# Performance work log

Hardware: AMD Instinct MI355X
Metric: run time of the kernel (lower is better)

The kernel has to match this reference:

```python
import jax, jax.numpy as jnp
import numpy as np

B, NQ, NK = 4, 2048, 2048
D_MODEL, D_K, D_V, H = 1024, 1024, 1024, 16


def setup_inputs() -> dict:
    key = jax.random.key(0)
    ks = jax.random.split(key, 8)
    return {
        "queries": jax.random.normal(ks[0], (B, NQ, D_MODEL), dtype=jnp.float32),
        "keys": jax.random.normal(ks[1], (B, NK, D_MODEL), dtype=jnp.float32),
        "values": jax.random.normal(ks[2], (B, NK, D_MODEL), dtype=jnp.float32),
        # nn.Linear weights init.normal_(std=0.001); stored here in (in, out) layout
        "Wq": jax.random.normal(ks[3], (D_MODEL, D_K), dtype=jnp.float32) * 0.001,
        "Wk": jax.random.normal(ks[4], (D_MODEL, D_K), dtype=jnp.float32) * 0.001,
        "Wv": jax.random.normal(ks[5], (D_MODEL, D_V), dtype=jnp.float32) * 0.001,
        "Wo": jax.random.normal(ks[6], (D_V, D_MODEL), dtype=jnp.float32) * 0.001,
        "bo": jnp.zeros((D_MODEL,), dtype=jnp.float32),
    }


def reference(queries, keys, values, Wq, Wk, Wv, Wo, bo):
    b_s, nq, _ = queries.shape
    nk = keys.shape[1]
    hd_k = D_K // H  # per-head key dim
    hd_v = D_V // H  # per-head value dim
    # projections -> [b, h, n, hd]
    q = (queries @ Wq).reshape(b_s, nq, H, hd_k).transpose(0, 2, 1, 3)
    k = (keys @ Wk).reshape(b_s, nk, H, hd_k).transpose(0, 2, 1, 3)
    v = (values @ Wv).reshape(b_s, nk, H, hd_v).transpose(0, 2, 1, 3)
    # NOTE: original scales by sqrt(d_k) (full d_k), not per-head dim
    att = jnp.einsum("bhqd,bhkd->bhqk", q, k) / np.float32(np.sqrt(D_K))
    att = jax.nn.softmax(att, axis=-1)
    # dropout = identity (eval mode)
    out = jnp.einsum("bhqk,bhkd->bhqd", att, v)
    out = out.transpose(0, 2, 1, 3).reshape(b_s, nq, D_V)
    return out @ Wo + bo
```

## Files before the change

kernel.cpp:

```cpp
#include <hip/hip_runtime.h>


#define DM    1024
#define NSEQ  2048
#define HEADS 16
#define HD    64

typedef float floatx4 __attribute__((ext_vector_type(4)));
typedef short s16x4   __attribute__((ext_vector_type(4)));
typedef short s16x8   __attribute__((ext_vector_type(8)));
typedef unsigned int u32x4 __attribute__((ext_vector_type(4)));

static __device__ __forceinline__ floatx4 mfma_bf16(s16x8 a, s16x8 b, floatx4 c) {
  return __builtin_amdgcn_mfma_f32_16x16x32_bf16(a, b, c, 0, 0, 0);
}

static __device__ __forceinline__ void gload_lds16(const void* g, void* l) {
  __builtin_amdgcn_global_load_lds(
      (const __attribute__((address_space(1))) unsigned*)g,
      (__attribute__((address_space(3))) unsigned*)l, 16, 0, 0);
}

static __device__ __forceinline__ unsigned lds_addr(const void* p) {
  return (unsigned)(unsigned long long)p;
}

static __device__ __forceinline__ s16x8 ds_read_b128a(unsigned byteaddr) {
  s16x8 r;
  asm volatile("ds_read_b128 %0, %1" : "=v"(r) : "v"(byteaddr));
  return r;
}

#define WAIT_LGKM0() \
  { asm volatile("s_waitcnt lgkmcnt(0)" ::: "memory"); __builtin_amdgcn_sched_barrier(0); }
#define WAIT_VMCNT(N) asm volatile("s_waitcnt vmcnt(" #N ")" ::: "memory")

static __device__ __forceinline__ short f2bf(float f) {
  unsigned u = __builtin_bit_cast(unsigned, f);
  u += 0x7FFFu + ((u >> 16) & 1u);
  return (short)(u >> 16);
}

static __device__ __forceinline__ unsigned cvtpk_bf16(float lo, float hi) {
  unsigned r;
  asm("v_cvt_pk_bf16_f32 %0, %1, %2" : "=v"(r) : "v"(lo), "v"(hi));
  return r;
}

static __device__ __forceinline__ unsigned pack2_bf16(float a, float b) {
  unsigned ua = __builtin_bit_cast(unsigned, a) + 0x8000u;
  unsigned ub = __builtin_bit_cast(unsigned, b) + 0x8000u;
#if __has_builtin(__builtin_amdgcn_perm)
  return __builtin_amdgcn_perm(ub, ua, 0x07060302u);
#else
  return (ub & 0xffff0000u) | (ua >> 16);
#endif
}

__global__ __launch_bounds__(256) void transpose_cast_w(
    const float* __restrict__ W0, const float* __restrict__ W1,
    const float* __restrict__ W2, const float* __restrict__ W3,
    short* __restrict__ T0, short* __restrict__ T1,
    short* __restrict__ T2, short* __restrict__ T3) {
  __shared__ float tile[32][33];
  const float* W = blockIdx.z == 0 ? W0 : blockIdx.z == 1 ? W1 : blockIdx.z == 2 ? W2 : W3;
  short*       T = blockIdx.z == 0 ? T0 : blockIdx.z == 1 ? T1 : blockIdx.z == 2 ? T2 : T3;
  const int bx = blockIdx.x * 32;
  const int by = blockIdx.y * 32;
  const int tx = threadIdx.x, ty = threadIdx.y;
  for (int i = 0; i < 4; i++)
    tile[ty + i * 8][tx] = W[(long)(by + ty + i * 8) * DM + bx + tx];
  __syncthreads();
  for (int i = 0; i < 4; i++)
    T[(long)(bx + ty + i * 8) * DM + by + tx] = f2bf(tile[tx][ty + i * 8]);
}

__global__ __launch_bounds__(256, 2) void proj_kernel(
    const float* __restrict__ Aq, const float* __restrict__ Ak, const float* __restrict__ Av,
    const short* __restrict__ BtQ, const short* __restrict__ BtK, const short* __restrict__ BtV,
    short* __restrict__ Qh, short* __restrict__ Kh, short* __restrict__ Vt) {
  __shared__ short lds[3 * 12288];
  const int z = blockIdx.z;
  const float* A  = z == 0 ? Aq  : z == 1 ? Ak  : Av;
  const short* Bt = z == 0 ? BtQ : z == 1 ? BtK : BtV;
  const int t = threadIdx.x;
  const int w = t >> 6, l = t & 63, quad = l >> 4, lm = l & 15;
  const int wm = w >> 1, wn = w & 1;
  const int row0 = blockIdx.x * 128, col0 = blockIdx.y * 128;

  floatx4 acc[4][4];
  for (int mi = 0; mi < 4; mi++)
    for (int ni = 0; ni < 4; ni++) acc[mi][ni] = (floatx4){0.f, 0.f, 0.f, 0.f};

  auto stage = [&](int k0, int buf) __attribute__((always_inline)) {
    short* base = lds + buf * 12288;
#pragma unroll
    for (int i = 0; i < 4; i++) {
      int g = w * 4 + i;
      const float* src =
          A + (long)(row0 + ((g >> 1) << 4) + lm) * DM + k0 + quad * 8 + (g & 1) * 4;
      gload_lds16(src, base + g * 512);
    }
#pragma unroll
    for (int i = 0; i < 2; i++) {
      int gb = w * 2 + i;
      const short* src = Bt + (long)(col0 + gb * 16 + lm) * DM + k0 + quad * 8;
      gload_lds16(src, base + 8192 + gb * 512);
    }
  };

  const unsigned lds0 = lds_addr(lds);
  auto process = [&](int buf) __attribute__((always_inline)) {
    const unsigned lbase = lds0 + buf * 24576;
    const unsigned abase = lbase + wm * 8192 + l * 16;
    const unsigned bbase = lbase + 16384 + wn * 4096 + l * 16;
    floatx4 alo[4], ahi[4];
    s16x8 bfr[4];
#pragma unroll
    for (int mi = 0; mi < 4; mi++) {
      alo[mi] = __builtin_bit_cast(floatx4, ds_read_b128a(abase + (mi * 2) * 1024));
      ahi[mi] = __builtin_bit_cast(floatx4, ds_read_b128a(abase + (mi * 2 + 1) * 1024));
    }
#pragma unroll
    for (int ni = 0; ni < 4; ni++)
      bfr[ni] = ds_read_b128a(bbase + ni * 1024);
    WAIT_LGKM0();
    s16x8 af[4];
#pragma unroll
    for (int mi = 0; mi < 4; mi++) {
      u32x4 p = {cvtpk_bf16(alo[mi][0], alo[mi][1]), cvtpk_bf16(alo[mi][2], alo[mi][3]),
                 cvtpk_bf16(ahi[mi][0], ahi[mi][1]), cvtpk_bf16(ahi[mi][2], ahi[mi][3])};
      af[mi] = __builtin_bit_cast(s16x8, p);
    }
    __builtin_amdgcn_s_setprio(1);
#pragma unroll
    for (int mi = 0; mi < 4; mi++)
#pragma unroll
      for (int ni = 0; ni < 4; ni++)
        acc[mi][ni] = mfma_bf16(af[mi], bfr[ni], acc[mi][ni]);
    __builtin_amdgcn_s_setprio(0);
  };

  stage(0, 0);
  stage(32, 1);
  int cur = 0;
  for (int tt = 0; tt < 30; ++tt) {
    WAIT_VMCNT(6);
    __builtin_amdgcn_s_barrier();
    __builtin_amdgcn_sched_barrier(0);
    int nb = cur + 2 >= 3 ? cur - 1 : cur + 2;
    stage((tt + 2) * 32, nb);
    __builtin_amdgcn_sched_barrier(0);
    process(cur);
    cur = cur + 1 >= 3 ? 0 : cur + 1;
  }
  WAIT_VMCNT(6);
  __builtin_amdgcn_s_barrier();
  __builtin_amdgcn_sched_barrier(0);
  process(cur);
  cur = cur + 1 >= 3 ? 0 : cur + 1;
  WAIT_VMCNT(0);
  __builtin_amdgcn_s_barrier();
  __builtin_amdgcn_sched_barrier(0);
  process(cur);

  const int rowbase = row0 + wm * 64;
  const int colbase = col0 + wn * 64;
  const int b = rowbase >> 11;
  const int h = colbase >> 6;
  const int rloc = rowbase & 2047;
  if (z < 2) {
    short* Out = z == 0 ? Qh : Kh;
    const float osc = z == 0 ? 0.0450842200277801f : 1.0f;
    long base = ((long)(b * HEADS + h)) * NSEQ * HD;
    for (int mi = 0; mi < 4; mi++)
      for (int r = 0; r < 4; r++) {
        int q = rloc + mi * 16 + quad * 4 + r;
        long rowoff = base + (long)q * HD + lm;
        for (int ni = 0; ni < 4; ni++)
          Out[rowoff + ni * 16] = f2bf(acc[mi][ni][r] * osc);
      }
  } else {
    long base = ((long)(b * HEADS + h)) * HD * NSEQ;
    for (int mi = 0; mi < 4; mi++)
      for (int r = 0; r < 4; r++) {
        int kcol = rloc + (mi >> 1) * 32 + quad * 8 + (mi & 1) * 4 + r;
        for (int ni = 0; ni < 4; ni++)
          Vt[base + (long)(ni * 16 + lm) * NSEQ + kcol] = f2bf(acc[mi][ni][r]);
      }
  }
}

__global__ __launch_bounds__(256, 2) void attn_kernel(
    const short* __restrict__ Qh, const short* __restrict__ Kh,
    const short* __restrict__ Vt, short* __restrict__ Obf) {
  __shared__ short lds[2 * 8192];
  const int t = threadIdx.x;
  const int w = t >> 6, l = t & 63, quad = l >> 4, lm = l & 15;
  const int bh = blockIdx.x;
  const int qtile = blockIdx.y * 128 + w * 32;
  const short* Qp = Qh + (long)bh * NSEQ * HD;
  const short* Kp = Kh + (long)bh * NSEQ * HD;
  const short* Vp = Vt + (long)bh * HD * NSEQ;

  s16x8 aq[2][2];
#pragma unroll
  for (int qi = 0; qi < 2; qi++)
#pragma unroll
    for (int c = 0; c < 2; c++)
      aq[qi][c] = *(const s16x8*)(Qp + (long)(qtile + qi * 16 + lm) * HD + c * 32 + quad * 8);

  floatx4 acc[2][4];
  float lsum[2] = {0.f, 0.f};
#pragma unroll
  for (int qi = 0; qi < 2; qi++)
#pragma unroll
    for (int n = 0; n < 4; n++) acc[qi][n] = (floatx4){0.f, 0.f, 0.f, 0.f};

  auto stage = [&](int kt, int buf) __attribute__((always_inline)) {
    short* base = lds + buf * 8192;
#pragma unroll
    for (int i = 0; i < 4; i++) {
      int g = w * 4 + i;
      const short* src;
      if (w < 2) {
        int s = (g >> 2) & 1, j = (g >> 1) & 1, c = g & 1;
        src = Kp + (long)(kt + s * 32 + j * 16 + lm) * HD + c * 32 + quad * 8;
      } else {
        int gg = g & 7;
        int s = gg >> 2, n = gg & 3;
        src = Vp + (long)(n * 16 + lm) * NSEQ + kt + s * 32 + quad * 8;
      }
      gload_lds16(src, base + g * 512);
    }
  };

  auto process = [&](const short* Lb, int s) __attribute__((always_inline)) {
    s16x8 bk[2][2];
#pragma unroll
    for (int j = 0; j < 2; j++)
#pragma unroll
      for (int c = 0; c < 2; c++)
        bk[j][c] = *(const s16x8*)(Lb + ((s * 4 + j * 2 + c) * 64 + l) * 8);
    s16x8 vraw[4];
#pragma unroll
    for (int n = 0; n < 4; n++)
      vraw[n] = *(const s16x8*)(Lb + ((8 + s * 4 + n) * 64 + l) * 8);
#pragma unroll
    for (int qi = 0; qi < 2; qi++) {
      floatx4 sT[2];
      sT[0] = (floatx4){0.f, 0.f, 0.f, 0.f};
      sT[1] = (floatx4){0.f, 0.f, 0.f, 0.f};
      __builtin_amdgcn_s_setprio(1);
#pragma unroll
      for (int c = 0; c < 2; c++) {
        sT[0] = mfma_bf16(bk[0][c], aq[qi][c], sT[0]);
        sT[1] = mfma_bf16(bk[1][c], aq[qi][c], sT[1]);
      }
      __builtin_amdgcn_s_setprio(0);
      float p0 = __builtin_amdgcn_exp2f(sT[0][0]);
      float p1 = __builtin_amdgcn_exp2f(sT[0][1]);
      float p2 = __builtin_amdgcn_exp2f(sT[0][2]);
      float p3 = __builtin_amdgcn_exp2f(sT[0][3]);
      float p4 = __builtin_amdgcn_exp2f(sT[1][0]);
      float p5 = __builtin_amdgcn_exp2f(sT[1][1]);
      float p6 = __builtin_amdgcn_exp2f(sT[1][2]);
      float p7 = __builtin_amdgcn_exp2f(sT[1][3]);
      lsum[qi] += ((p0 + p1) + (p2 + p3)) + ((p4 + p5) + (p6 + p7));
      u32x4 pw = {pack2_bf16(p0, p1), pack2_bf16(p2, p3),
                  pack2_bf16(p4, p5), pack2_bf16(p6, p7)};
      s16x8 pcat = __builtin_bit_cast(s16x8, pw);
      __builtin_amdgcn_s_setprio(1);
#pragma unroll
      for (int n = 0; n < 4; n++)
        acc[qi][n] = mfma_bf16(vraw[n], pcat, acc[qi][n]);
      __builtin_amdgcn_s_setprio(0);
    }
  };

  stage(0, 0);
  __syncthreads();
  int cur = 0;
  for (int kt = 0; kt < NSEQ; kt += 64) {
    if (kt + 64 < NSEQ) stage(kt + 64, cur ^ 1);
    const short* Lb = lds + cur * 8192;
    process(Lb, 0);
    process(Lb, 1);
    __syncthreads();
    cur ^= 1;
  }

  const int b = bh >> 4, h = bh & 15;
  short* Ow = lds + w * 1152;
  const int erow = l >> 2, ecg = l & 3;
#pragma unroll
  for (int qi = 0; qi < 2; qi++) {
    float ls = lsum[qi];
    ls += __shfl_xor(ls, 16);
    ls += __shfl_xor(ls, 32);
    float rl = 1.0f / ls;
#pragma unroll
    for (int n = 0; n < 4; n++)
#pragma unroll
      for (int r = 0; r < 4; r++)
        Ow[lm * 72 + n * 16 + quad * 4 + r] = f2bf(acc[qi][n][r] * rl);
    s16x8 o0 = *(const s16x8*)(Ow + erow * 72 + ecg * 16);
    s16x8 o1 = *(const s16x8*)(Ow + erow * 72 + ecg * 16 + 8);
    long gaddr = ((long)(b * NSEQ + qtile + qi * 16 + erow)) * DM + h * HD + ecg * 16;
    *(s16x8*)(Obf + gaddr) = o0;
    *(s16x8*)(Obf + gaddr + 8) = o1;
  }
}

__global__ __launch_bounds__(256, 2) void out_kernel(
    const short* __restrict__ Ab, const short* __restrict__ Bt,
    const float* __restrict__ bias, float* __restrict__ Out) {
  __shared__ short lds[3 * 8192];
  const int t = threadIdx.x;
  const int w = t >> 6, l = t & 63, quad = l >> 4, lm = l & 15;
  const int wm = w >> 1, wn = w & 1;
  const int row0 = blockIdx.x * 128, col0 = blockIdx.y * 128;

  floatx4 acc[4][4];
  for (int mi = 0; mi < 4; mi++)
    for (int ni = 0; ni < 4; ni++) acc[mi][ni] = (floatx4){0.f, 0.f, 0.f, 0.f};

  auto stage = [&](int k0, int buf) __attribute__((always_inline)) {
    short* base = lds + buf * 8192;
#pragma unroll
    for (int i = 0; i < 4; i++) {
      int g = w * 4 + i;
      const short* src = (g < 8)
          ? Ab + (long)(row0 + g * 16 + lm) * DM + k0 + quad * 8
          : Bt + (long)(col0 + (g - 8) * 16 + lm) * DM + k0 + quad * 8;
      gload_lds16(src, base + g * 512);
    }
  };
  const unsigned lds0 = lds_addr(lds);
  auto process = [&](int buf) __attribute__((always_inline)) {
    const unsigned lbase = lds0 + buf * 16384;
    const unsigned abase = lbase + wm * 4096 + l * 16;
    const unsigned bbase = lbase + 8192 + wn * 4096 + l * 16;
    s16x8 af[4], bfr[4];
#pragma unroll
    for (int mi = 0; mi < 4; mi++)
      af[mi] = ds_read_b128a(abase + mi * 1024);
#pragma unroll
    for (int ni = 0; ni < 4; ni++)
      bfr[ni] = ds_read_b128a(bbase + ni * 1024);
    WAIT_LGKM0();
    __builtin_amdgcn_s_setprio(1);
#pragma unroll
    for (int mi = 0; mi < 4; mi++)
#pragma unroll
      for (int ni = 0; ni < 4; ni++)
        acc[mi][ni] = mfma_bf16(af[mi], bfr[ni], acc[mi][ni]);
    __builtin_amdgcn_s_setprio(0);
  };

  stage(0, 0);
  stage(32, 1);
  int cur = 0;
  for (int tt = 0; tt < 30; ++tt) {
    WAIT_VMCNT(4);
    __builtin_amdgcn_s_barrier();
    __builtin_amdgcn_sched_barrier(0);
    int nb = cur + 2 >= 3 ? cur - 1 : cur + 2;
    stage((tt + 2) * 32, nb);
    __builtin_amdgcn_sched_barrier(0);
    process(cur);
    cur = cur + 1 >= 3 ? 0 : cur + 1;
  }
  WAIT_VMCNT(4);
  __builtin_amdgcn_s_barrier();
  __builtin_amdgcn_sched_barrier(0);
  process(cur);
  cur = cur + 1 >= 3 ? 0 : cur + 1;
  WAIT_VMCNT(0);
  __builtin_amdgcn_s_barrier();
  __builtin_amdgcn_sched_barrier(0);
  process(cur);

  const int rowbase = row0 + wm * 64;
  const int colbase = col0 + wn * 64;
  for (int mi = 0; mi < 4; mi++)
    for (int r = 0; r < 4; r++) {
      int gr = rowbase + mi * 16 + quad * 4 + r;
      for (int ni = 0; ni < 4; ni++) {
        int gc = colbase + ni * 16 + lm;
        Out[(long)gr * DM + gc] = acc[mi][ni][r] + bias[gc];
      }
    }
}

extern "C" void kernel_launch(void* const* d_in, const int* in_sizes, int n_in,
                              void* d_out, int out_size, void* d_ws, size_t ws_size,
                              hipStream_t stream) {
  (void)in_sizes; (void)n_in; (void)out_size; (void)ws_size;
  const float* queries = (const float*)d_in[0];
  const float* keys    = (const float*)d_in[1];
  const float* values  = (const float*)d_in[2];
  const float* Wq = (const float*)d_in[3];
  const float* Wk = (const float*)d_in[4];
  const float* Wv = (const float*)d_in[5];
  const float* Wo = (const float*)d_in[6];
  const float* bo = (const float*)d_in[7];
  float* out = (float*)d_out;

  char* ws = (char*)d_ws;
  const size_t MB = 1024 * 1024;
  short* WqT = (short*)(ws + 0 * MB);
  short* WkT = (short*)(ws + 2 * MB);
  short* WvT = (short*)(ws + 4 * MB);
  short* WoT = (short*)(ws + 6 * MB);
  short* Qh  = (short*)(ws + 8 * MB);
  short* Kh  = (short*)(ws + 24 * MB);
  short* Vt  = (short*)(ws + 40 * MB);
  short* Obf = (short*)(ws + 56 * MB);

  transpose_cast_w<<<dim3(32, 32, 4), dim3(32, 8), 0, stream>>>(
      Wq, Wk, Wv, Wo, WqT, WkT, WvT, WoT);
  proj_kernel<<<dim3(64, 8, 3), 256, 0, stream>>>(
      queries, keys, values, WqT, WkT, WvT, Qh, Kh, Vt);
  attn_kernel<<<dim3(64, 16), 256, 0, stream>>>(Qh, Kh, Vt, Obf);
  out_kernel<<<dim3(64, 8), 256, 0, stream>>>(Obf, WoT, bo, out);
}
```

Baseline: 388.3 us.

## Use 64-wide K steps with double buffering and wider proj tiles

The projection GEMM moves to 512-thread blocks with 128x256 tiles and 64-wide K steps. It swaps the triple-buffered vmcnt-gated pipeline for a plain double buffer with __syncthreads. The output GEMM and the attention kernel also double their per-stage K chunk (64 and 128 keys) so there are half as many barriers and loop iterations. The cost is much more LDS per block (128KB for proj), which may reduce occupancy. The simpler full-barrier sync also loses the finer-grained overlap of the previous vmcnt scheme.

Result: faster. 374.7 us (-3.5%).

```diff
diff --git a/kernel.cpp b/kernel.cpp
--- a/kernel.cpp
+++ b/kernel.cpp
@@ -33,7 +33,6 @@
 
 #define WAIT_LGKM0() \
   { asm volatile("s_waitcnt lgkmcnt(0)" ::: "memory"); __builtin_amdgcn_sched_barrier(0); }
-#define WAIT_VMCNT(N) asm volatile("s_waitcnt vmcnt(" #N ")" ::: "memory")
 
 static __device__ __forceinline__ short f2bf(float f) {
   unsigned u = __builtin_bit_cast(unsigned, f);
@@ -75,94 +74,86 @@
     T[(long)(bx + ty + i * 8) * DM + by + tx] = f2bf(tile[tx][ty + i * 8]);
 }
 
-__global__ __launch_bounds__(256, 2) void proj_kernel(
+__global__ __launch_bounds__(512, 2) void proj_kernel(
     const float* __restrict__ Aq, const float* __restrict__ Ak, const float* __restrict__ Av,
     const short* __restrict__ BtQ, const short* __restrict__ BtK, const short* __restrict__ BtV,
     short* __restrict__ Qh, short* __restrict__ Kh, short* __restrict__ Vt) {
-  __shared__ short lds[3 * 12288];
+  __shared__ short lds[2 * 32768];
   const int z = blockIdx.z;
   const float* A  = z == 0 ? Aq  : z == 1 ? Ak  : Av;
   const short* Bt = z == 0 ? BtQ : z == 1 ? BtK : BtV;
   const int t = threadIdx.x;
   const int w = t >> 6, l = t & 63, quad = l >> 4, lm = l & 15;
-  const int wm = w >> 1, wn = w & 1;
-  const int row0 = blockIdx.x * 128, col0 = blockIdx.y * 128;
+  const int wm = w >> 2, wn = w & 3;
+  const int row0 = blockIdx.x * 128, col0 = blockIdx.y * 256;
 
   floatx4 acc[4][4];
   for (int mi = 0; mi < 4; mi++)
     for (int ni = 0; ni < 4; ni++) acc[mi][ni] = (floatx4){0.f, 0.f, 0.f, 0.f};
 
   auto stage = [&](int k0, int buf) __attribute__((always_inline)) {
-    short* base = lds + buf * 12288;
+    short* base = lds + buf * 32768;
 #pragma unroll
     for (int i = 0; i < 4; i++) {
-      int g = w * 4 + i;
+      int ga = w * 4 + i, g16 = ga >> 2, kk = (ga >> 1) & 1, h = ga & 1;
       const float* src =
-          A + (long)(row0 + ((g >> 1) << 4) + lm) * DM + k0 + quad * 8 + (g & 1) * 4;
-      gload_lds16(src, base + g * 512);
-    }
-#pragma unroll
-    for (int i = 0; i < 2; i++) {
-      int gb = w * 2 + i;
-      const short* src = Bt + (long)(col0 + gb * 16 + lm) * DM + k0 + quad * 8;
-      gload_lds16(src, base + 8192 + gb * 512);
+          A + (long)(row0 + g16 * 16 + lm) * DM + k0 + kk * 32 + quad * 8 + h * 4;
+      gload_lds16(src, base + ga * 512);
+    }
+#pragma unroll
+    for (int i = 0; i < 4; i++) {
+      int gb = w * 4 + i, g16c = gb >> 1, kk = gb & 1;
+      const short* src =
+          Bt + (long)(col0 + g16c * 16 + lm) * DM + k0 + kk * 32 + quad * 8;
+      gload_lds16(src, base + 16384 + gb * 512);
     }
   };
 
   const unsigned lds0 = lds_addr(lds);
   auto process = [&](int buf) __attribute__((always_inline)) {
-    const unsigned lbase = lds0 + buf * 24576;
-    const unsigned abase = lbase + wm * 8192 + l * 16;
-    const unsigned bbase = lbase + 16384 + wn * 4096 + l * 16;
-    floatx4 alo[4], ahi[4];
-    s16x8 bfr[4];
-#pragma unroll
-    for (int mi = 0; mi < 4; mi++) {
-      alo[mi] = __builtin_bit_cast(floatx4, ds_read_b128a(abase + (mi * 2) * 1024));
-      ahi[mi] = __builtin_bit_cast(floatx4, ds_read_b128a(abase + (mi * 2 + 1) * 1024));
-    }
-#pragma unroll
-    for (int ni = 0; ni < 4; ni++)
-      bfr[ni] = ds_read_b128a(bbase + ni * 1024);
-    WAIT_LGKM0();
-    s16x8 af[4];
-#pragma unroll
-    for (int mi = 0; mi < 4; mi++) {
-      u32x4 p = {cvtpk_bf16(alo[mi][0], alo[mi][1]), cvtpk_bf16(alo[mi][2], alo[mi][3]),
-                 cvtpk_bf16(ahi[mi][0], ahi[mi][1]), cvtpk_bf16(ahi[mi][2], ahi[mi][3])};
-      af[mi] = __builtin_bit_cast(s16x8, p);
-    }
-    __builtin_amdgcn_s_setprio(1);
-#pragma unroll
-    for (int mi = 0; mi < 4; mi++)
-#pragma unroll
-      for (int ni = 0; ni < 4; ni++)
-        acc[mi][ni] = mfma_bf16(af[mi], bfr[ni], acc[mi][ni]);
-    __builtin_amdgcn_s_setprio(0);
+    const unsigned lbase = lds0 + buf * 65536;
+#pragma unroll
+    for (int kk = 0; kk < 2; kk++) {
+      floatx4 alo[4], ahi[4];
+      s16x8 bfr[4];
+#pragma unroll
+      for (int mi = 0; mi < 4; mi++) {
+        unsigned ga0 = ((wm * 4 + mi) * 4 + kk * 2) * 1024;
+        alo[mi] = __builtin_bit_cast(floatx4, ds_read_b128a(lbase + ga0 + l * 16));
+        ahi[mi] = __builtin_bit_cast(floatx4, ds_read_b128a(lbase + ga0 + 1024 + l * 16));
+      }
+#pragma unroll
+      for (int ni = 0; ni < 4; ni++) {
+        unsigned gb0 = 32768u + ((wn * 4 + ni) * 2 + kk) * 1024;
+        bfr[ni] = ds_read_b128a(lbase + gb0 + l * 16);
+      }
+      WAIT_LGKM0();
+      s16x8 af[4];
+#pragma unroll
+      for (int mi = 0; mi < 4; mi++) {
+        u32x4 p = {cvtpk_bf16(alo[mi][0], alo[mi][1]), cvtpk_bf16(alo[mi][2], alo[mi][3]),
+                   cvtpk_bf16(ahi[mi][0], ahi[mi][1]), cvtpk_bf16(ahi[mi][2], ahi[mi][3])};
+        af[mi] = __builtin_bit_cast(s16x8, p);
+      }
+      __builtin_amdgcn_s_setprio(1);
+#pragma unroll
+      for (int mi = 0; mi < 4; mi++)
+#pragma unroll
+        for (int ni = 0; ni < 4; ni++)
+          acc[mi][ni] = mfma_bf16(af[mi], bfr[ni], acc[mi][ni]);
+      __builtin_amdgcn_s_setprio(0);
+    }
   };
 
   stage(0, 0);
-  stage(32, 1);
+  __syncthreads();
   int cur = 0;
-  for (int tt = 0; tt < 30; ++tt) {
-    WAIT_VMCNT(6);
-    __builtin_amdgcn_s_barrier();
-    __builtin_amdgcn_sched_barrier(0);
-    int nb = cur + 2 >= 3 ? cur - 1 : cur + 2;
-    stage((tt + 2) * 32, nb);
-    __builtin_amdgcn_sched_barrier(0);
+  for (int tt = 0; tt < 16; ++tt) {
+    if (tt + 1 < 16) stage((tt + 1) * 64, cur ^ 1);
     process(cur);
-    cur = cur + 1 >= 3 ? 0 : cur + 1;
+    __syncthreads();
+    cur ^= 1;
   }
-  WAIT_VMCNT(6);
-  __builtin_amdgcn_s_barrier();
-  __builtin_amdgcn_sched_barrier(0);
-  process(cur);
-  cur = cur + 1 >= 3 ? 0 : cur + 1;
-  WAIT_VMCNT(0);
-  __builtin_amdgcn_s_barrier();
-  __builtin_amdgcn_sched_barrier(0);
-  process(cur);
 
   const int rowbase = row0 + wm * 64;
   const int colbase = col0 + wn * 64;
@@ -194,7 +185,7 @@
 __global__ __launch_bounds__(256, 2) void attn_kernel(
     const short* __restrict__ Qh, const short* __restrict__ Kh,
     const short* __restrict__ Vt, short* __restrict__ Obf) {
-  __shared__ short lds[2 * 8192];
+  __shared__ short lds[2 * 16384];
   const int t = threadIdx.x;
   const int w = t >> 6, l = t & 63, quad = l >> 4, lm = l & 15;
   const int bh = blockIdx.x;
@@ -218,16 +209,16 @@
     for (int n = 0; n < 4; n++) acc[qi][n] = (floatx4){0.f, 0.f, 0.f, 0.f};
 
   auto stage = [&](int kt, int buf) __attribute__((always_inline)) {
-    short* base = lds + buf * 8192;
-#pragma unroll
-    for (int i = 0; i < 4; i++) {
-      int g = w * 4 + i;
+    short* base = lds + buf * 16384;
+#pragma unroll
+    for (int i = 0; i < 8; i++) {
+      int g = w * 8 + i;
       const short* src;
       if (w < 2) {
-        int s = (g >> 2) & 1, j = (g >> 1) & 1, c = g & 1;
+        int s = g >> 2, j = (g >> 1) & 1, c = g & 1;
         src = Kp + (long)(kt + s * 32 + j * 16 + lm) * HD + c * 32 + quad * 8;
       } else {
-        int gg = g & 7;
+        int gg = g & 15;
         int s = gg >> 2, n = gg & 3;
         src = Vp + (long)(n * 16 + lm) * NSEQ + kt + s * 32 + quad * 8;
       }
@@ -245,7 +236,7 @@
     s16x8 vraw[4];
 #pragma unroll
     for (int n = 0; n < 4; n++)
-      vraw[n] = *(const s16x8*)(Lb + ((8 + s * 4 + n) * 64 + l) * 8);
+      vraw[n] = *(const s16x8*)(Lb + ((16 + s * 4 + n) * 64 + l) * 8);
 #pragma unroll
     for (int qi = 0; qi < 2; qi++) {
       floatx4 sT[2];
@@ -281,11 +272,13 @@
   stage(0, 0);
   __syncthreads();
   int cur = 0;
-  for (int kt = 0; kt < NSEQ; kt += 64) {
-    if (kt + 64 < NSEQ) stage(kt + 64, cur ^ 1);
-    const short* Lb = lds + cur * 8192;
+  for (int kt = 0; kt < NSEQ; kt += 128) {
+    if (kt + 128 < NSEQ) stage(kt + 128, cur ^ 1);
+    const short* Lb = lds + cur * 16384;
     process(Lb, 0);
     process(Lb, 1);
+    process(Lb, 2);
+    process(Lb, 3);
     __syncthreads();
     cur ^= 1;
   }
@@ -315,7 +308,7 @@
 __global__ __launch_bounds__(256, 2) void out_kernel(
     const short* __restrict__ Ab, const short* __restrict__ Bt,
     const float* __restrict__ bias, float* __restrict__ Out) {
-  __shared__ short lds[3 * 8192];
+  __shared__ short lds[2 * 16384];
   const int t = threadIdx.x;
   const int w = t >> 6, l = t & 63, quad = l >> 4, lm = l & 15;
   const int wm = w >> 1, wn = w & 1;
@@ -326,60 +319,56 @@
     for (int ni = 0; ni < 4; ni++) acc[mi][ni] = (floatx4){0.f, 0.f, 0.f, 0.f};
 
   auto stage = [&](int k0, int buf) __attribute__((always_inline)) {
-    short* base = lds + buf * 8192;
-#pragma unroll
-    for (int i = 0; i < 4; i++) {
-      int g = w * 4 + i;
-      const short* src = (g < 8)
-          ? Ab + (long)(row0 + g * 16 + lm) * DM + k0 + quad * 8
-          : Bt + (long)(col0 + (g - 8) * 16 + lm) * DM + k0 + quad * 8;
-      gload_lds16(src, base + g * 512);
+    short* base = lds + buf * 16384;
+#pragma unroll
+    for (int i = 0; i < 8; i++) {
+      int g = w * 8 + i;
+      const short* src;
+      short* dst;
+      if (g < 16) {
+        int g16 = g >> 1, kk = g & 1;
+        src = Ab + (long)(row0 + g16 * 16 + lm) * DM + k0 + kk * 32 + quad * 8;
+        dst = base + g * 512;
+      } else {
+        int gb = g - 16, g16 = gb >> 1, kk = gb & 1;
+        src = Bt + (long)(col0 + g16 * 16 + lm) * DM + k0 + kk * 32 + quad * 8;
+        dst = base + 8192 + gb * 512;
+      }
+      gload_lds16(src, dst);
     }
   };
   const unsigned lds0 = lds_addr(lds);
   auto process = [&](int buf) __attribute__((always_inline)) {
-    const unsigned lbase = lds0 + buf * 16384;
-    const unsigned abase = lbase + wm * 4096 + l * 16;
-    const unsigned bbase = lbase + 8192 + wn * 4096 + l * 16;
-    s16x8 af[4], bfr[4];
-#pragma unroll
-    for (int mi = 0; mi < 4; mi++)
-      af[mi] = ds_read_b128a(abase + mi * 1024);
-#pragma unroll
-    for (int ni = 0; ni < 4; ni++)
-      bfr[ni] = ds_read_b128a(bbase + ni * 1024);
-    WAIT_LGKM0();
-    __builtin_amdgcn_s_setprio(1);
-#pragma unroll
-    for (int mi = 0; mi < 4; mi++)
+    const unsigned lbase = lds0 + buf * 32768;
+#pragma unroll
+    for (int kk = 0; kk < 2; kk++) {
+      s16x8 af[4], bfr[4];
+#pragma unroll
+      for (int mi = 0; mi < 4; mi++)
+        af[mi] = ds_read_b128a(lbase + ((wm * 4 + mi) * 2 + kk) * 1024 + l * 16);
 #pragma unroll
       for (int ni = 0; ni < 4; ni++)
-        acc[mi][ni] = mfma_bf16(af[mi], bfr[ni], acc[mi][ni]);
-    __builtin_amdgcn_s_setprio(0);
+        bfr[ni] = ds_read_b128a(lbase + 16384 + ((wn * 4 + ni) * 2 + kk) * 1024 + l * 16);
+      WAIT_LGKM0();
+      __builtin_amdgcn_s_setprio(1);
+#pragma unroll
+      for (int mi = 0; mi < 4; mi++)
+#pragma unroll
+        for (int ni = 0; ni < 4; ni++)
+          acc[mi][ni] = mfma_bf16(af[mi], bfr[ni], acc[mi][ni]);
+      __builtin_amdgcn_s_setprio(0);
+    }
   };
 
   stage(0, 0);
-  stage(32, 1);
+  __syncthreads();
   int cur = 0;
-  for (int tt = 0; tt < 30; ++tt) {
-    WAIT_VMCNT(4);
-    __builtin_amdgcn_s_barrier();
-    __builtin_amdgcn_sched_barrier(0);
-    int nb = cur + 2 >= 3 ? cur - 1 : cur + 2;
-    stage((tt + 2) * 32, nb);
-    __builtin_amdgcn_sched_barrier(0);
+  for (int tt = 0; tt < 16; ++tt) {
+    if (tt + 1 < 16) stage((tt + 1) * 64, cur ^ 1);
     process(cur);
-    cur = cur + 1 >= 3 ? 0 : cur + 1;
+    __syncthreads();
+    cur ^= 1;
   }
-  WAIT_VMCNT(4);
-  __builtin_amdgcn_s_barrier();
-  __builtin_amdgcn_sched_barrier(0);
-  process(cur);
-  cur = cur + 1 >= 3 ? 0 : cur + 1;
-  WAIT_VMCNT(0);
-  __builtin_amdgcn_s_barrier();
-  __builtin_amdgcn_sched_barrier(0);
-  process(cur);
 
   const int rowbase = row0 + wm * 64;
   const int colbase = col0 + wn * 64;
@@ -420,7 +409,7 @@
 
   transpose_cast_w<<<dim3(32, 32, 4), dim3(32, 8), 0, stream>>>(
       Wq, Wk, Wv, Wo, WqT, WkT, WvT, WoT);
-  proj_kernel<<<dim3(64, 8, 3), 256, 0, stream>>>(
+  proj_kernel<<<dim3(64, 4, 3), 512, 0, stream>>>(
       queries, keys, values, WqT, WkT, WvT, Qh, Kh, Vt);
   attn_kernel<<<dim3(64, 16), 256, 0, stream>>>(Qh, Kh, Vt, Obf);
   out_kernel<<<dim3(64, 8), 256, 0, stream>>>(Obf, WoT, bo, out);
```
